# Kernel tuning notes

Hardware: AMD Instinct MI355X
Metric: run time of the kernel (lower is better)

The kernel has to match this reference:

```python
import jax, jax.numpy as jnp
import numpy as np

B, C, H8, W8 = 2, 256, 56, 96
RADIUS, LEVELS = 4, 4


def setup_inputs() -> dict:
    key = jax.random.key(0)
    k1, k2, k3, k4, k5 = jax.random.split(key, 5)
    fmap1 = jax.random.normal(k1, (B, C, H8, W8), jnp.float32)
    fmap2 = jax.random.normal(k2, (B, C, H8, W8), jnp.float32)
    xs = jnp.arange(W8, dtype=jnp.float32)
    ys = jnp.arange(H8, dtype=jnp.float32)
    bx, by = jnp.broadcast_arrays(xs[None, :], ys[:, None])
    base = jnp.stack([bx, by], axis=0)  # [2,H8,W8], x first (as create_coords_grid)
    coords = base[None] + 4.0 * jax.random.normal(k3, (B, 2, H8, W8), jnp.float32)
    flow = jax.random.normal(k4, (B, 2, H8, W8), jnp.float32)
    mask = jax.random.normal(k5, (B, 9 * 8 * 8, H8, W8), jnp.float32)
    return {"fmap1": fmap1, "fmap2": fmap2, "coords": coords, "flow": flow, "mask": mask}


def _bilinear_sample(cflat, Hl, Wl, px, py):
    # cflat: [N, Hl*Wl]; px,py: [N,P] pixel coords; zero padding outside (grid_sample default)
    x0 = jnp.floor(px)
    y0 = jnp.floor(py)
    wx = px - x0
    wy = py - y0
    x0 = x0.astype(jnp.int32)
    y0 = y0.astype(jnp.int32)

    def g(xi, yi):
        valid = (xi >= 0) & (xi <= Wl - 1) & (yi >= 0) & (yi <= Hl - 1)
        idx = jnp.clip(yi, 0, Hl - 1) * Wl + jnp.clip(xi, 0, Wl - 1)
        return jnp.where(valid, jnp.take_along_axis(cflat, idx, axis=1), 0.0)

    return ((1 - wy) * ((1 - wx) * g(x0, y0) + wx * g(x0 + 1, y0))
            + wy * ((1 - wx) * g(x0, y0 + 1) + wx * g(x0 + 1, y0 + 1)))


def _corr_lookup(fmap1, fmap2, coords):
    b, c, h, w = fmap1.shape
    n = b * h * w
    # all-pairs correlation, scaled by sqrt(C)
    corr = jnp.einsum('bchw,bcij->bhwij', fmap1, fmap2) / jnp.sqrt(jnp.float32(c))
    cl = corr.reshape(n, h, w)
    # query coords (pixel units at level 0)
    cx = coords[:, 0].reshape(n)
    cy = coords[:, 1].reshape(n)
    r = RADIUS
    lin = jnp.linspace(-r, r, 2 * r + 1, dtype=jnp.float32)
    # replicates torch.meshgrid(dy,dx) quirk: x-offset varies along axis 0, y along axis 1
    xo = jnp.repeat(lin, 2 * r + 1)  # [81]
    yo = jnp.tile(lin, 2 * r + 1)    # [81]
    outs = []
    for i in range(LEVELS):
        Hl, Wl = cl.shape[1], cl.shape[2]
        cflat = cl.reshape(n, Hl * Wl)
        px = cx[:, None] / (2 ** i) + xo[None, :]
        py = cy[:, None] / (2 ** i) + yo[None, :]
        samp = _bilinear_sample(cflat, Hl, Wl, px, py)  # [N,81]
        outs.append(samp.reshape(b, h, w, -1))
        if i < LEVELS - 1:  # 2x2 avg pool, stride 2
            cl = cl.reshape(n, Hl // 2, 2, Wl // 2, 2).mean(axis=(2, 4))
    out = jnp.concatenate(outs, axis=-1)  # [B,h,w,4*81]
    return out.transpose(0, 3, 1, 2)


def _convex_upsample(flow, mask):
    b, ch, h, w = flow.shape
    m = mask.reshape(b, 1, 9, 8, 8, h, w)
    m = jax.nn.softmax(m, axis=2)
    fp = jnp.pad(8.0 * flow, ((0, 0), (0, 0), (1, 1), (1, 1)))
    # 3x3 unfold, kernel positions row-major (matches F.unfold ordering)
    patches = jnp.stack([fp[:, :, i:i + h, j:j + w]
                         for i in range(3) for j in range(3)], axis=2)  # [B,2,9,h,w]
    up = jnp.sum(m * patches[:, :, :, None, None], axis=2)  # [B,2,8,8,h,w]
    up = up.transpose(0, 1, 4, 2, 5, 3)  # [B,2,h,8,w,8]
    return up.reshape(b, ch, 8 * h, 8 * w)


def reference(fmap1, fmap2, coords, flow, mask):
    corr_feats = _corr_lookup(fmap1, fmap2, coords)  # [B,324,H8,W8]
    up_flow = _convex_upsample(flow, mask)           # [B,2,8*H8,8*W8]
    return (corr_feats, up_flow)
```

## Files before the change

### kernel.cpp

```cpp
#include <hip/hip_runtime.h>
#include <math.h>

constexpr int B = 2, C = 256, H = 56, W = 96;
constexpr int HW = H * W;

#define SQ 21.166666f
constexpr float SCL = 36.0f / (127.0f * 127.0f * 16.0f);

constexpr size_t F1T_B = 0;
constexpr size_t L0_B  = (size_t)B * HW * C;
constexpr size_t L1_B  = L0_B + (size_t)B * HW * C;
constexpr size_t L2_B  = L1_B + (size_t)B * 28 * 48 * C;
constexpr size_t L3_B  = L2_B + (size_t)B * 14 * 24 * C;
constexpr size_t STG_B = L3_B + (size_t)B * 7 * 12 * C;
constexpr size_t OUT0_ELEMS = (size_t)B * 324 * HW;

static __device__ __forceinline__ int dot4acc(int a, int b, int c) {
#if __has_builtin(__builtin_amdgcn_sdot4)
    return __builtin_amdgcn_sdot4(a, b, c, false);
#else
    c += (int)(char)(a) * (int)(char)(b);
    c += (int)(char)(a >> 8) * (int)(char)(b >> 8);
    c += (int)(char)(a >> 16) * (int)(char)(b >> 16);
    c += (int)(char)(a >> 24) * (int)(char)(b >> 24);
    return c;
#endif
}

static __device__ __forceinline__ unsigned short pack_i8x2(float a, float b) {
    int ia = (int)rintf(a); ia = ia < -127 ? -127 : (ia > 127 ? 127 : ia);
    int ib = (int)rintf(b); ib = ib < -127 ? -127 : (ib > 127 ? 127 : ib);
    return (unsigned short)((ia & 0xFF) | ((ib & 0xFF) << 8));
}

__global__ void transpose_in(const float* __restrict__ fmap1,
                             const float* __restrict__ fmap2,
                             char* __restrict__ ws) {
    __shared__ float tile[64][33];
    int z = blockIdx.z;
    int b = z & 1, m = z >> 1;
    const float* src = m ? fmap2 : fmap1;
    unsigned short* dst = (unsigned short*)(ws + (m ? L0_B : F1T_B));
    int c0 = blockIdx.y * 64, q0 = blockIdx.x * 32;
    int tx = threadIdx.x, ty = threadIdx.y;
#pragma unroll
    for (int r = 0; r < 8; ++r) {
        int cl = ty + r * 8;
        tile[cl][tx] = src[((size_t)(b * C + c0 + cl)) * HW + q0 + tx];
    }
    __syncthreads();
#pragma unroll
    for (int r = 0; r < 4; ++r) {
        int pl = ty + r * 8;
        dst[((size_t)b * HW + q0 + pl) * 128 + (c0 >> 1) + tx] =
            pack_i8x2(tile[2 * tx][pl] * SQ, tile[2 * tx + 1][pl] * SQ);
    }
}

constexpr int NP1 = B * 28 * 48 * C / 2;
constexpr int NP2 = B * 14 * 24 * C / 2;
constexpr int NP3 = B * 7 * 12 * C / 2;
__global__ void build_pools(char* __restrict__ ws) {
    const unsigned short* L0p = (const unsigned short*)(ws + L0_B);
    int t = blockIdx.x * 256 + threadIdx.x;
    int l, tl;
    if (t < NP1)             { l = 1; tl = t; }
    else if (t < NP1 + NP2)  { l = 2; tl = t - NP1; }
    else                     { l = 3; tl = t - NP1 - NP2; }
    int Wo = W >> l, Ho = H >> l, S = 1 << l;
    int c2 = tl & 127;
    int r = tl >> 7;
    int x = r % Wo; r /= Wo;
    int y = r % Ho;
    int b = r / Ho;
    int sx = 0, sy = 0;
    for (int dy = 0; dy < S; ++dy)
        for (int dx = 0; dx < S; ++dx) {
            unsigned short v = L0p[((size_t)(b * H + y * S + dy) * W + x * S + dx) * 128 + c2];
            sx += (int)(char)(v & 0xFF);
            sy += (int)(char)(v >> 8);
        }
    float inv = 1.0f / (S * S);
    unsigned short* dst = (unsigned short*)(ws + (l == 1 ? L1_B : (l == 2 ? L2_B : L3_B)));
    dst[tl] = pack_i8x2((float)sx * inv, (float)sy * inv);
}

__global__ __launch_bounds__(256) void corr_lookup(
    const float* __restrict__ coords, const char* __restrict__ ws,
    _Float16* __restrict__ stage) {
    int q = blockIdx.x;
    int b = q & 1;
    int pos = q >> 1;
    int w = pos % W;
    int h = pos / W;
    int tid = threadIdx.x;

    __shared__ float Dsh[4][100];

    int wave = tid >> 6, lane = tid & 63, u = lane & 7, grp = lane >> 3;

    const int4* ap = (const int4*)(ws + F1T_B + ((size_t)b * HW + h * W + w) * C);
    int4 A0 = ap[2 * u], A1 = ap[2 * u + 1];

    int l = wave;
    int Hl = H >> l, Wl = W >> l;
    size_t off = (l == 0 ? L0_B : (l == 1 ? L1_B : (l == 2 ? L2_B : L3_B)));
    const char* base8 = ws + off + (size_t)b * Hl * Wl * C;

    float cx = coords[((size_t)(b * 2 + 0)) * HW + h * W + w];
    float cy = coords[((size_t)(b * 2 + 1)) * HW + h * W + w];
    float scale = 1.0f / (float)(1 << l);
    float fx = cx * scale, fy = cy * scale;
    float fxf = floorf(fx), fyf = floorf(fy);
    float wx = fx - fxf, wy = fy - fyf;
    int ix = (int)fxf, iy = (int)fyf;

    int xx = grp;
    int x = ix - 4 + grp;
    int y = iy - 4;

#pragma unroll
    for (int it = 0; it < 13; ++it) {
        bool live = (it < 12) | (grp < 4);
        int s = 0;
        if (live && (unsigned)x < (unsigned)Wl && (unsigned)y < (unsigned)Hl) {
            const int4* cp = (const int4*)(base8 + ((size_t)(y * Wl + x)) * C + u * 32);
            int4 c0 = cp[0], c1 = cp[1];
            s = dot4acc(c0.x, A0.x, s);
            s = dot4acc(c0.y, A0.y, s);
            s = dot4acc(c0.z, A0.z, s);
            s = dot4acc(c0.w, A0.w, s);
            s = dot4acc(c1.x, A1.x, s);
            s = dot4acc(c1.y, A1.y, s);
            s = dot4acc(c1.z, A1.z, s);
            s = dot4acc(c1.w, A1.w, s);
        }
        s += __shfl_xor(s, 1);
        s += __shfl_xor(s, 2);
        s += __shfl_xor(s, 4);
        if (u == 0 && live) Dsh[wave][it * 8 + grp] = (float)s * SCL;
        xx += 8;
        int carry = (xx >= 10);
        xx -= carry ? 10 : 0;
        x += carry ? -2 : 8;
        y += carry;
    }
    __syncthreads();

    size_t bse = ((size_t)b * HW + h * W + w) * 324 + l * 81;
    for (int o = lane; o < 81; o += 64) {
        int xo = o / 9;
        int yo = o - xo * 9;
        float v00 = Dsh[wave][yo * 10 + xo];
        float v01 = Dsh[wave][yo * 10 + xo + 1];
        float v10 = Dsh[wave][(yo + 1) * 10 + xo];
        float v11 = Dsh[wave][(yo + 1) * 10 + xo + 1];
        float s = (1.f - wy) * ((1.f - wx) * v00 + wx * v01)
                +        wy  * ((1.f - wx) * v10 + wx * v11);
        stage[bse + o] = (_Float16)s;
    }
}

constexpr int T_BLOCKS = 168 * 11 * B;
__global__ __launch_bounds__(256) void tail_kernel(
    const _Float16* __restrict__ stage, const float* __restrict__ flow,
    const float* __restrict__ mask, float* __restrict__ out0,
    float* __restrict__ out1) {
    __shared__ float smem[72 * 96 + 2 * 3 * 98];
    int blk = blockIdx.x;
    int tid = threadIdx.x;

    if (blk < T_BLOCKS) {
        float (*tile)[33] = (float(*)[33])smem;
        int b = blk / (168 * 11);
        int rem = blk % (168 * 11);
        int by = rem / 168, bx = rem % 168;
        int ch0 = by * 32, q0 = bx * 32;
        int tx = tid & 31, ty = tid >> 5;
#pragma unroll
        for (int r = 0; r < 4; ++r) {
            int pl = ty + r * 8;
            if (ch0 + tx < 324)
                tile[pl][tx] = (float)stage[((size_t)b * HW + q0 + pl) * 324 + ch0 + tx];
        }
        __syncthreads();
#pragma unroll
        for (int r = 0; r < 4; ++r) {
            int chl = ty + r * 8;
            if (ch0 + chl < 324)
                out0[((size_t)(b * 324 + ch0 + chl)) * HW + q0 + tx] = tile[tx][chl];
        }
        return;
    }

    float* msk = smem;
    float* fst = smem + 72 * 96;
    int cb = blk - T_BLOCKS;
    int i = cb & 7;
    int r = cb >> 3;
    int h = r % H;
    int b = r / H;

    for (int idx = tid; idx < 72 * 96; idx += 256) {
        int row = idx / 96, wc = idx - row * 96;
        int k = row >> 3, j = row & 7;
        int gl = k * 64 + i * 8 + j;
        msk[idx] = mask[((size_t)(b * 576 + gl)) * HW + h * W + wc];
    }
    for (int idx = tid; idx < 588; idx += 256) {
        int ch = idx / 294;
        int rem2 = idx - ch * 294;
        int rr = rem2 / 98;
        int xw = rem2 - rr * 98;
        int hh = h + rr - 1, ww = xw - 1;
        float v = 0.f;
        if (hh >= 0 && hh < H && ww >= 0 && ww < W)
            v = 8.0f * flow[((size_t)(b * 2 + ch)) * HW + hh * W + ww];
        fst[idx] = v;
    }
    __syncthreads();

#pragma unroll
    for (int rr = 0; rr < 3; ++rr) {
        int col = tid + rr * 256;
        int w = col >> 3, j = col & 7;
        float m[9], mx = -1e30f;
#pragma unroll
        for (int k = 0; k < 9; ++k) {
            m[k] = msk[(k * 8 + j) * 96 + w];
            mx = fmaxf(mx, m[k]);
        }
        float sum = 0.f;
#pragma unroll
        for (int k = 0; k < 9; ++k) {
            m[k] = __expf(m[k] - mx);
            sum += m[k];
        }
        float inv = 1.0f / sum;
        float a0 = 0.f, a1 = 0.f;
#pragma unroll
        for (int k = 0; k < 9; ++k) {
            int ki = k / 3, kj = k - ki * 3;
            float wgt = m[k] * inv;
            a0 = fmaf(wgt, fst[0 * 294 + ki * 98 + w + kj], a0);
            a1 = fmaf(wgt, fst[1 * 294 + ki * 98 + w + kj], a1);
        }
        size_t row8 = (size_t)8 * h + i;
        out1[((size_t)(b * 2 + 0) * 448 + row8) * 768 + col] = a0;
        out1[((size_t)(b * 2 + 1) * 448 + row8) * 768 + col] = a1;
    }
}

extern "C" void kernel_launch(void* const* d_in, const int* in_sizes, int n_in,
                              void* d_out, int out_size, void* d_ws, size_t ws_size,
                              hipStream_t stream) {
    const float* fmap1  = (const float*)d_in[0];
    const float* fmap2  = (const float*)d_in[1];
    const float* coords = (const float*)d_in[2];
    const float* flow   = (const float*)d_in[3];
    const float* maskp  = (const float*)d_in[4];
    float* out = (float*)d_out;
    char* ws = (char*)d_ws;
    _Float16* stage = (_Float16*)(ws + STG_B);

    transpose_in<<<dim3(HW / 32, C / 64, 2 * B), dim3(32, 8), 0, stream>>>(fmap1, fmap2, ws);
    build_pools<<<(NP1 + NP2 + NP3) / 256, 256, 0, stream>>>(ws);
    corr_lookup<<<B * HW, 256, 0, stream>>>(coords, ws, stage);
    tail_kernel<<<T_BLOCKS + B * H * 8, 256, 0, stream>>>(stage, flow, maskp, out, out + OUT0_ELEMS);
}
```

Before: 158.9 us.

## Compute local correlation window with int8 MFMA instead of sdot4 and shuffles

Replaces the per-lane sdot4 dot products and cross-lane shuffle reductions with MFMA 16x16x64 int8 matrix ops. Each of 16 rows holds one window position's fmap2 feature vector, and the fmap1 vector is placed only in column 0 of B. This removes the shuffle reduction, but most of the MFMA output columns are wasted because only one is useful. Invalid positions are clamped to in-range addresses and masked out with a ballot.

```diff
diff --git a/kernel.cpp b/kernel.cpp
--- a/kernel.cpp
+++ b/kernel.cpp
@@ -6,6 +6,8 @@
 
 #define SQ 21.166666f
 constexpr float SCL = 36.0f / (127.0f * 127.0f * 16.0f);
+
+typedef int int4v __attribute__((ext_vector_type(4)));
 
 constexpr size_t F1T_B = 0;
 constexpr size_t L0_B  = (size_t)B * HW * C;
@@ -14,18 +16,6 @@
 constexpr size_t L3_B  = L2_B + (size_t)B * 14 * 24 * C;
 constexpr size_t STG_B = L3_B + (size_t)B * 7 * 12 * C;
 constexpr size_t OUT0_ELEMS = (size_t)B * 324 * HW;
-
-static __device__ __forceinline__ int dot4acc(int a, int b, int c) {
-#if __has_builtin(__builtin_amdgcn_sdot4)
-    return __builtin_amdgcn_sdot4(a, b, c, false);
-#else
-    c += (int)(char)(a) * (int)(char)(b);
-    c += (int)(char)(a >> 8) * (int)(char)(b >> 8);
-    c += (int)(char)(a >> 16) * (int)(char)(b >> 16);
-    c += (int)(char)(a >> 24) * (int)(char)(b >> 24);
-    return c;
-#endif
-}
 
 static __device__ __forceinline__ unsigned short pack_i8x2(float a, float b) {
     int ia = (int)rintf(a); ia = ia < -127 ? -127 : (ia > 127 ? 127 : ia);
@@ -97,10 +87,18 @@
 
     __shared__ float Dsh[4][100];
 
-    int wave = tid >> 6, lane = tid & 63, u = lane & 7, grp = lane >> 3;
-
-    const int4* ap = (const int4*)(ws + F1T_B + ((size_t)b * HW + h * W + w) * C);
-    int4 A0 = ap[2 * u], A1 = ap[2 * u + 1];
+    int wave = tid >> 6, lane = tid & 63;
+    int m = lane & 15;
+    int kg = lane >> 4;
+
+    const int4v* f1p = (const int4v*)(ws + F1T_B + ((size_t)b * HW + h * W + w) * C);
+    int4v zero = {0, 0, 0, 0};
+    int4v Bf[4];
+#pragma unroll
+    for (int c = 0; c < 4; ++c) {
+        int4v v = f1p[c * 4 + kg];
+        Bf[c] = (m == 0) ? v : zero;
+    }
 
     int l = wave;
     int Hl = H >> l, Wl = W >> l;
@@ -115,35 +113,42 @@
     float wx = fx - fxf, wy = fy - fyf;
     int ix = (int)fxf, iy = (int)fyf;
 
-    int xx = grp;
-    int x = ix - 4 + grp;
-    int y = iy - 4;
-
-#pragma unroll
-    for (int it = 0; it < 13; ++it) {
-        bool live = (it < 12) | (grp < 4);
-        int s = 0;
-        if (live && (unsigned)x < (unsigned)Wl && (unsigned)y < (unsigned)Hl) {
-            const int4* cp = (const int4*)(base8 + ((size_t)(y * Wl + x)) * C + u * 32);
-            int4 c0 = cp[0], c1 = cp[1];
-            s = dot4acc(c0.x, A0.x, s);
-            s = dot4acc(c0.y, A0.y, s);
-            s = dot4acc(c0.z, A0.z, s);
-            s = dot4acc(c0.w, A0.w, s);
-            s = dot4acc(c1.x, A1.x, s);
-            s = dot4acc(c1.y, A1.y, s);
-            s = dot4acc(c1.z, A1.z, s);
-            s = dot4acc(c1.w, A1.w, s);
-        }
-        s += __shfl_xor(s, 1);
-        s += __shfl_xor(s, 2);
-        s += __shfl_xor(s, 4);
-        if (u == 0 && live) Dsh[wave][it * 8 + grp] = (float)s * SCL;
-        xx += 8;
+    int xx = m % 10;
+    int yy = m / 10;
+
+#pragma unroll
+    for (int c = 0; c < 7; ++c) {
+        int p = c * 16 + m;
+        int x = ix - 4 + xx;
+        int y = iy - 4 + yy;
+        bool valid = ((unsigned)x < (unsigned)Wl) & ((unsigned)y < (unsigned)Hl) & (p < 100);
+        int xc = min(max(x, 0), Wl - 1);
+        int yc = min(max(y, 0), Hl - 1);
+        const int4v* cp = (const int4v*)(base8 + ((size_t)(yc * Wl + xc)) * 256 + kg * 16);
+        int4v A0 = cp[0];
+        int4v A1 = cp[4];
+        int4v A2 = cp[8];
+        int4v A3 = cp[12];
+        unsigned long long msk = __ballot(valid);
+        int4v d;
+        d = __builtin_amdgcn_mfma_i32_16x16x64_i8(A0, Bf[0], zero, 0, 0, 0);
+        d = __builtin_amdgcn_mfma_i32_16x16x64_i8(A1, Bf[1], d, 0, 0, 0);
+        d = __builtin_amdgcn_mfma_i32_16x16x64_i8(A2, Bf[2], d, 0, 0, 0);
+        d = __builtin_amdgcn_mfma_i32_16x16x64_i8(A3, Bf[3], d, 0, 0, 0);
+        if (m == 0) {
+#pragma unroll
+            for (int r = 0; r < 4; ++r) {
+                int row = kg * 4 + r;
+                int pp = c * 16 + row;
+                if (pp < 100)
+                    Dsh[wave][pp] = ((msk >> row) & 1) ? (float)d[r] * SCL : 0.f;
+            }
+        }
+        xx += 6;
+        yy += 1;
         int carry = (xx >= 10);
         xx -= carry ? 10 : 0;
-        x += carry ? -2 : 8;
-        y += carry;
+        yy += carry;
     }
     __syncthreads();
 
```

After: 246.7 us. +55.3%, slower.

## Batch all neighbor loads before dot products and use DPP for group reduction

Applied to the files above, without the earlier changes.

The corr_lookup loop now issues all 13 iterations of int8 feature loads into register arrays first, then does the sdot4 accumulation in a second loop. This lets many global loads be in flight at once instead of serialising load-then-compute per iteration. The dot products use two accumulators to shorten dependency chains, and the 8-lane reduction uses DPP moves instead of shuffles. It raises register pressure (104 extra VGPRs for the load buffers), which may lower occupancy.

```diff
diff --git a/kernel.cpp b/kernel.cpp
--- a/kernel.cpp
+++ b/kernel.cpp
@@ -6,6 +6,8 @@
 
 #define SQ 21.166666f
 constexpr float SCL = 36.0f / (127.0f * 127.0f * 16.0f);
+
+typedef int int4v __attribute__((ext_vector_type(4)));
 
 constexpr size_t F1T_B = 0;
 constexpr size_t L0_B  = (size_t)B * HW * C;
@@ -24,6 +26,20 @@
     c += (int)(char)(a >> 16) * (int)(char)(b >> 16);
     c += (int)(char)(a >> 24) * (int)(char)(b >> 24);
     return c;
+#endif
+}
+
+static __device__ __forceinline__ int group8_sum(int s) {
+#if __has_builtin(__builtin_amdgcn_mov_dpp)
+    s += __builtin_amdgcn_mov_dpp(s, 0xB1, 0xF, 0xF, true);
+    s += __builtin_amdgcn_mov_dpp(s, 0x4E, 0xF, 0xF, true);
+    s += __builtin_amdgcn_mov_dpp(s, 0x141, 0xF, 0xF, true);
+    return s;
+#else
+    s += __shfl_xor(s, 1);
+    s += __shfl_xor(s, 2);
+    s += __shfl_xor(s, 4);
+    return s;
 #endif
 }
 
@@ -99,8 +115,8 @@
 
     int wave = tid >> 6, lane = tid & 63, u = lane & 7, grp = lane >> 3;
 
-    const int4* ap = (const int4*)(ws + F1T_B + ((size_t)b * HW + h * W + w) * C);
-    int4 A0 = ap[2 * u], A1 = ap[2 * u + 1];
+    const int4v* ap = (const int4v*)(ws + F1T_B + ((size_t)b * HW + h * W + w) * C);
+    int4v A0 = ap[2 * u], A1 = ap[2 * u + 1];
 
     int l = wave;
     int Hl = H >> l, Wl = W >> l;
@@ -119,31 +135,40 @@
     int x = ix - 4 + grp;
     int y = iy - 4;
 
+    int4v Lo[13], Hi[13];
+    const int4v zero = {0, 0, 0, 0};
+
 #pragma unroll
     for (int it = 0; it < 13; ++it) {
         bool live = (it < 12) | (grp < 4);
-        int s = 0;
+        Lo[it] = zero;
+        Hi[it] = zero;
         if (live && (unsigned)x < (unsigned)Wl && (unsigned)y < (unsigned)Hl) {
-            const int4* cp = (const int4*)(base8 + ((size_t)(y * Wl + x)) * C + u * 32);
-            int4 c0 = cp[0], c1 = cp[1];
-            s = dot4acc(c0.x, A0.x, s);
-            s = dot4acc(c0.y, A0.y, s);
-            s = dot4acc(c0.z, A0.z, s);
-            s = dot4acc(c0.w, A0.w, s);
-            s = dot4acc(c1.x, A1.x, s);
-            s = dot4acc(c1.y, A1.y, s);
-            s = dot4acc(c1.z, A1.z, s);
-            s = dot4acc(c1.w, A1.w, s);
-        }
-        s += __shfl_xor(s, 1);
-        s += __shfl_xor(s, 2);
-        s += __shfl_xor(s, 4);
-        if (u == 0 && live) Dsh[wave][it * 8 + grp] = (float)s * SCL;
+            const int4v* cp = (const int4v*)(base8 + ((size_t)(y * Wl + x)) * C + u * 32);
+            Lo[it] = cp[0];
+            Hi[it] = cp[1];
+        }
         xx += 8;
         int carry = (xx >= 10);
         xx -= carry ? 10 : 0;
         x += carry ? -2 : 8;
         y += carry;
+    }
+
+#pragma unroll
+    for (int it = 0; it < 13; ++it) {
+        bool live = (it < 12) | (grp < 4);
+        int s0 = 0, s1 = 0;
+        s0 = dot4acc(Lo[it].x, A0.x, s0);
+        s1 = dot4acc(Lo[it].y, A0.y, s1);
+        s0 = dot4acc(Lo[it].z, A0.z, s0);
+        s1 = dot4acc(Lo[it].w, A0.w, s1);
+        s0 = dot4acc(Hi[it].x, A1.x, s0);
+        s1 = dot4acc(Hi[it].y, A1.y, s1);
+        s0 = dot4acc(Hi[it].z, A1.z, s0);
+        s1 = dot4acc(Hi[it].w, A1.w, s1);
+        int s = group8_sum(s0 + s1);
+        if (u == 0 && live) Dsh[wave][it * 8 + grp] = (float)s * SCL;
     }
     __syncthreads();
 
```

Result: no change. 158.0 us (-0.6%).
